# Performance work log

Hardware: AMD Instinct MI355X
Metric: run time of the kernel (lower is better)

Reference implementation:

```python
import jax, jax.numpy as jnp
import numpy as np

B, S, D, H, DFF = 8, 1024, 1024, 16, 4096
DK = D // H
EPS = 1e-6
NEG = -1e9


def setup_inputs() -> dict:
    key = jax.random.key(0)
    ks = jax.random.split(key, 8)
    x = jax.random.normal(ks[0], (B, S, D), dtype=jnp.float32)
    mask = jnp.ones((B, 1, 1, S), dtype=jnp.int32)
    s = 0.02
    wq = jax.random.normal(ks[1], (D, D), jnp.float32) * s
    wk = jax.random.normal(ks[2], (D, D), jnp.float32) * s
    wv = jax.random.normal(ks[3], (D, D), jnp.float32) * s
    wo = jax.random.normal(ks[4], (D, D), jnp.float32) * s
    bq = jnp.zeros((D,), jnp.float32); bk = jnp.zeros((D,), jnp.float32)
    bv = jnp.zeros((D,), jnp.float32); bo = jnp.zeros((D,), jnp.float32)
    w1 = jax.random.normal(ks[5], (D, DFF), jnp.float32) * s
    b1 = jnp.zeros((DFF,), jnp.float32)
    w2 = jax.random.normal(ks[6], (DFF, D), jnp.float32) * s
    b2 = jnp.zeros((D,), jnp.float32)
    g1 = jnp.array(1.0, jnp.float32); be1 = jnp.array(0.0, jnp.float32)
    g2 = jnp.array(1.0, jnp.float32); be2 = jnp.array(0.0, jnp.float32)
    return dict(x=x, mask=mask, wq=wq, bq=bq, wk=wk, bk=bk, wv=wv, bv=bv,
                wo=wo, bo=bo, w1=w1, b1=b1, w2=w2, b2=b2,
                g1=g1, be1=be1, g2=g2, be2=be2)


def layer_norm(x, gamma, beta):
    # repo quirk: unbiased std (ddof=1), scalar gamma/beta, divide by (std+eps)
    mean = jnp.mean(x, axis=-1, keepdims=True)
    std = jnp.std(x, axis=-1, keepdims=True, ddof=1)
    return gamma * (x - mean) / (std + EPS) + beta


def mha(x, mask, wq, bq, wk, bk, wv, bv, wo, bo):
    q = (x @ wq + bq).reshape(B, S, H, DK).transpose(0, 2, 1, 3)  # bhsd
    k = (x @ wk + bk).reshape(B, S, H, DK).transpose(0, 2, 1, 3)
    v = (x @ wv + bv).reshape(B, S, H, DK).transpose(0, 2, 1, 3)
    scores = jnp.einsum('bhqd,bhkd->bhqk', q, k) / jnp.sqrt(jnp.float32(DK))
    scores = jnp.where(mask == 0, NEG, scores)
    attn = jax.nn.softmax(scores, axis=-1)
    out = jnp.einsum('bhqk,bhkd->bhqd', attn, v)
    out = out.transpose(0, 2, 1, 3).reshape(B, S, D)
    return out @ wo + bo


def reference(x, mask, wq, bq, wk, bk, wv, bv, wo, bo, w1, b1, w2, b2, g1, be1, g2, be2):
    # pre-LN residual: x + sublayer(norm(x)); dropout inert at eval
    x = x + mha(layer_norm(x, g1, be1), mask, wq, bq, wk, bk, wv, bv, wo, bo)
    h = layer_norm(x, g2, be2)
    x = x + (jax.nn.relu(h @ w1 + b1) @ w2 + b2)
    return x
```

## Files before the change

### kernel.cpp

```cpp
#include <hip/hip_runtime.h>
#include <math.h>

typedef __bf16 bf16;
typedef float f32x4 __attribute__((ext_vector_type(4)));
typedef float f32x16 __attribute__((ext_vector_type(16)));
typedef bf16 bf16x8 __attribute__((ext_vector_type(8)));
typedef bf16 bf16x4 __attribute__((ext_vector_type(4)));
typedef unsigned int u32;
typedef unsigned int u32x2 __attribute__((ext_vector_type(2)));

#define DEV __device__ __forceinline__

constexpr int Ss = 1024, Dd = 1024;
constexpr float EPSf = 1e-6f;
constexpr float SM_SCALE = 0.125f * 1.4426950408889634f;

DEV void gl_lds16(const void* g, void* l) {
  __builtin_amdgcn_global_load_lds(
      (const __attribute__((address_space(1))) void*)g,
      (__attribute__((address_space(3))) void*)l, 16, 0, 0);
}

DEV u32 cvtpk(float lo, float hi) {
  u32 r;
  asm("v_cvt_pk_bf16_f32 %0, %1, %2" : "=v"(r) : "v"(lo), "v"(hi));
  return r;
}

__global__ __launch_bounds__(256) void prep_k(
    const float* __restrict__ i0, const float* __restrict__ i1,
    const float* __restrict__ i2, const float* __restrict__ i3,
    const float* __restrict__ i4, const float* __restrict__ i5,
    bf16* __restrict__ o0, bf16* __restrict__ o1, bf16* __restrict__ o2,
    bf16* __restrict__ o3, bf16* __restrict__ o4, bf16* __restrict__ o5,
    const float* __restrict__ xin, bf16* __restrict__ lnout,
    const float* __restrict__ gp, const float* __restrict__ bp) {
  const int bi = blockIdx.x;
  const int tid = threadIdx.x;
  if (bi >= 3072) {
    const int row = bi - 3072;
    float v[4];
    const float* p = xin + (size_t)row * Dd + tid * 4;
#pragma unroll
    for (int i = 0; i < 4; i++) v[i] = p[i];
    float s = v[0] + v[1] + v[2] + v[3];
    float s2 = v[0] * v[0] + v[1] * v[1] + v[2] * v[2] + v[3] * v[3];
#pragma unroll
    for (int m = 1; m < 64; m <<= 1) {
      s += __shfl_xor(s, m, 64);
      s2 += __shfl_xor(s2, m, 64);
    }
    __shared__ float ls[4], ls2[4];
    if ((tid & 63) == 0) {
      ls[tid >> 6] = s;
      ls2[tid >> 6] = s2;
    }
    __syncthreads();
    s = ls[0] + ls[1] + ls[2] + ls[3];
    s2 = ls2[0] + ls2[1] + ls2[2] + ls2[3];
    float mean = s * (1.0f / Dd);
    float var = (s2 - (float)Dd * mean * mean) * (1.0f / (Dd - 1));
    var = fmaxf(var, 0.0f);
    float g = gp[0], be = bp[0];
    float rs = g / (sqrtf(var) + EPSf);
    bf16* q = lnout + (size_t)row * Dd + tid * 4;
#pragma unroll
    for (int i = 0; i < 4; i++) q[i] = (bf16)((v[i] - mean) * rs + be);
    return;
  }
  __shared__ float t[64 * 65];
  const float* in;
  bf16* out;
  int R, C, local, sh;
  if (bi < 1024) {
    const int j = bi >> 8;
    local = bi & 255; R = 1024; C = 1024; sh = 4;
    in = (j == 0) ? i0 : (j == 1) ? i1 : (j == 2) ? i2 : i3;
    out = (j == 0) ? o0 : (j == 1) ? o1 : (j == 2) ? o2 : o3;
  } else if (bi < 2048) {
    local = bi - 1024; R = 1024; C = 4096; sh = 6; in = i4; out = o4;
  } else {
    local = bi - 2048; R = 4096; C = 1024; sh = 4; in = i5; out = o5;
  }
  const int nx = 1 << sh;
  const int bx = local & (nx - 1), by = local >> sh;
  const int tx = tid & 63, ty = tid >> 6;
  const int r0 = by * 64, c0 = bx * 64;
#pragma unroll
  for (int i = 0; i < 16; i++) {
    int r = ty + i * 4;
    t[r * 65 + tx] = in[(size_t)(r0 + r) * C + c0 + tx];
  }
  __syncthreads();
#pragma unroll
  for (int i = 0; i < 16; i++) {
    int r = ty + i * 4;
    out[(size_t)(c0 + r) * R + r0 + tx] = (bf16)t[tx * 65 + r];
  }
}

__global__ __launch_bounds__(256) void ln_kernel(
    const float* __restrict__ in, bf16* __restrict__ out,
    const float* __restrict__ gp, const float* __restrict__ bp) {
  const int row = blockIdx.x;
  const int tid = threadIdx.x;
  float v[4];
  const float* p = in + (size_t)row * Dd + tid * 4;
#pragma unroll
  for (int i = 0; i < 4; i++) v[i] = p[i];
  float s = v[0] + v[1] + v[2] + v[3];
  float s2 = v[0] * v[0] + v[1] * v[1] + v[2] * v[2] + v[3] * v[3];
#pragma unroll
  for (int m = 1; m < 64; m <<= 1) {
    s += __shfl_xor(s, m, 64);
    s2 += __shfl_xor(s2, m, 64);
  }
  __shared__ float ls[4], ls2[4];
  if ((tid & 63) == 0) {
    ls[tid >> 6] = s;
    ls2[tid >> 6] = s2;
  }
  __syncthreads();
  s = ls[0] + ls[1] + ls[2] + ls[3];
  s2 = ls2[0] + ls2[1] + ls2[2] + ls2[3];
  float mean = s * (1.0f / Dd);
  float var = (s2 - (float)Dd * mean * mean) * (1.0f / (Dd - 1));
  var = fmaxf(var, 0.0f);
  float g = gp[0], be = bp[0];
  float rs = g / (sqrtf(var) + EPSf);
  bf16* q = out + (size_t)row * Dd + tid * 4;
#pragma unroll
  for (int i = 0; i < 4; i++) q[i] = (bf16)((v[i] - mean) * rs + be);
}

template <int EPI, int BK>
__global__ __launch_bounds__(256) void gemm_bt(
    const bf16* __restrict__ A, const bf16* __restrict__ Bt,
    const float* __restrict__ bias, const float* __restrict__ bias2,
    const float* __restrict__ bias3, const float* __restrict__ resid,
    bf16* __restrict__ vtb, void* __restrict__ Cout, int M, int N, int K,
    int sa, int sb) {
  __shared__ __attribute__((aligned(16))) char smem[2 * 128 * BK * 2];
  bf16* As = (bf16*)smem;
  bf16* Bs = (bf16*)(smem + 128 * BK * 2);
  constexpr int CPR = BK / 8;
  constexpr int RPJ = 256 / CPR;
  constexpr int NJ = BK / 16;
  const int tid = threadIdx.x;
  const int ln = tid & 63;
  const int wv = tid >> 6;
  const int wm = wv >> 1, wn = wv & 1;
  const int quad = ln >> 4, l16 = ln & 15;
  const int l7 = l16 & 7;
  const int nxg = gridDim.x;
  const int d = blockIdx.y * nxg + blockIdx.x;
  const int sseq = d >> 3;
  const int bxr = sseq % nxg;
  const int byr = (d & 7) + 8 * (sseq / nxg);
  const int m0 = byr * 128, n0 = bxr * 128;

  f32x4 acc[4][4];
#pragma unroll
  for (int i = 0; i < 4; i++)
#pragma unroll
    for (int j = 0; j < 4; j++) acc[i][j] = {0.f, 0.f, 0.f, 0.f};

  const int sr = tid / CPR;
  const int sc = (tid & (CPR - 1)) ^ (sr & 7);
  const size_t abase = (size_t)(m0 + sr) * sa + sc * 8;
  const size_t bbase = (size_t)(n0 + sr) * sb + sc * 8;

  for (int k0 = 0; k0 < K; k0 += BK) {
#pragma unroll
    for (int j = 0; j < NJ; j++) {
      gl_lds16(A + abase + (size_t)(j * RPJ) * sa + k0,
               (char*)As + j * 4096 + wv * 1024);
      gl_lds16(Bt + bbase + (size_t)(j * RPJ) * sb + k0,
               (char*)Bs + j * 4096 + wv * 1024);
    }
    __syncthreads();
#pragma unroll
    for (int kh = 0; kh < BK / 32; kh++) {
      bf16x8 af[4], bfr[4];
#pragma unroll
      for (int mi = 0; mi < 4; mi++)
        af[mi] = *(const bf16x8*)&As[(wm * 64 + mi * 16 + l16) * BK +
                                     ((kh * 4 + quad) ^ l7) * 8];
#pragma unroll
      for (int ni = 0; ni < 4; ni++)
        bfr[ni] = *(const bf16x8*)&Bs[(wn * 64 + ni * 16 + l16) * BK +
                                      ((kh * 4 + quad) ^ l7) * 8];
#pragma unroll
      for (int mi = 0; mi < 4; mi++)
#pragma unroll
        for (int ni = 0; ni < 4; ni++)
          acc[mi][ni] = __builtin_amdgcn_mfma_f32_16x16x32_bf16(
              af[mi], bfr[ni], acc[mi][ni], 0, 0, 0);
    }
    __syncthreads();
  }

  if constexpr (EPI == 4) {
    if (n0 < 2048) {
#pragma unroll
      for (int mi = 0; mi < 4; mi++) {
        const int m = m0 + wm * 64 + mi * 16 + quad * 4;
#pragma unroll
        for (int ni = 0; ni < 4; ni++) {
          const int n = n0 + wn * 64 + ni * 16 + l16;
          const float bvl = (n < 1024) ? bias[n] : bias2[n - 1024];
#pragma unroll
          for (int r = 0; r < 4; r++)
            ((bf16*)Cout)[(size_t)(m + r) * N + n] =
                (bf16)(acc[mi][ni][r] + bvl);
        }
      }
    } else {
      bf16* T = (bf16*)smem;
#pragma unroll
      for (int mi = 0; mi < 4; mi++) {
        const int ml = wm * 64 + mi * 16 + quad * 4;
        const int c = ml >> 3, hf = (ml >> 2) & 1;
#pragma unroll
        for (int ni = 0; ni < 4; ni++) {
          const int nl = wn * 64 + ni * 16 + l16;
          const float bvl = bias3[(n0 - 2048) + nl];
          bf16x4 tv;
#pragma unroll
          for (int r = 0; r < 4; r++) tv[r] = (bf16)(acc[mi][ni][r] + bvl);
          *(bf16x4*)&T[nl * 128 + ((c ^ (nl & 15)) << 3) + (hf << 2)] = tv;
        }
      }
      __syncthreads();
      const size_t vbase =
          ((size_t)(m0 >> 10) * 1024 + (n0 - 2048)) * Ss + (m0 & 1023);
#pragma unroll
      for (int p = 0; p < 8; p++) {
        const int row = p * 16 + (tid >> 4);
        const int k = tid & 15;
        bf16x8 vv = *(const bf16x8*)&T[row * 128 + ((k ^ (row & 15)) << 3)];
        *(bf16x8*)&vtb[vbase + (size_t)row * Ss + k * 8] = vv;
      }
    }
  } else {
#pragma unroll
    for (int mi = 0; mi < 4; mi++) {
      const int m = m0 + wm * 64 + mi * 16 + quad * 4;
#pragma unroll
      for (int ni = 0; ni < 4; ni++) {
        const int n = n0 + wn * 64 + ni * 16 + l16;
        float bvl = 0.0f;
        if constexpr (EPI != 3) bvl = bias[n];
#pragma unroll
        for (int r = 0; r < 4; r++) {
          float val = acc[mi][ni][r] + bvl;
          const size_t idx = (size_t)(m + r) * N + n;
          if constexpr (EPI == 1) {
            ((float*)Cout)[idx] = val + resid[idx];
          } else if constexpr (EPI == 2) {
            ((bf16*)Cout)[idx] = (bf16)fmaxf(val, 0.0f);
          } else {
            ((float*)Cout)[idx] = val + resid[idx];
          }
        }
      }
    }
  }
}

__global__ __launch_bounds__(512) void gemm256_relu(
    const bf16* __restrict__ A, const bf16* __restrict__ Bt,
    const float* __restrict__ bias, bf16* __restrict__ Cout, int M, int N,
    int K, int sa, int sb) {
  __shared__ __attribute__((aligned(16))) char smem[131072];
  const int tid = threadIdx.x;
  const int ln = tid & 63;
  const int wv = tid >> 6;
  const int wm = wv >> 2, wn = wv & 3;
  const int quad = ln >> 4, l16 = ln & 15;
  const int l7 = l16 & 7;
  const int nxg = gridDim.x;
  const int d = blockIdx.y * nxg + blockIdx.x;
  const int sseq = d >> 3;
  const int bxr = sseq % nxg;
  const int byr = (d & 7) + 8 * (sseq / nxg);
  const int m0 = byr * 256, n0 = bxr * 256;

  f32x4 acc[8][4];
#pragma unroll
  for (int i = 0; i < 8; i++)
#pragma unroll
    for (int j = 0; j < 4; j++) acc[i][j] = {0.f, 0.f, 0.f, 0.f};

  const int sr = tid >> 3;
  const int sc = (tid & 7) ^ (sr & 7);
  const size_t abase = (size_t)(m0 + sr) * sa + sc * 8;
  const size_t bbase = (size_t)(n0 + sr) * sb + sc * 8;
  const int w8 = tid >> 6;

  const int nt = K >> 6;
  int cur = 0;

  {
#pragma unroll
    for (int j = 0; j < 4; j++) {
      gl_lds16(A + abase + (size_t)(j * 64) * sa,
               smem + j * 8192 + w8 * 1024);
      gl_lds16(Bt + bbase + (size_t)(j * 64) * sb,
               smem + 32768 + j * 8192 + w8 * 1024);
    }
  }
  asm volatile("s_waitcnt vmcnt(0)" ::: "memory");
  __builtin_amdgcn_s_barrier();

  for (int t = 0; t < nt; ++t) {
    const bf16* As = (const bf16*)(smem + cur * 65536);
    const bf16* Bs = (const bf16*)(smem + cur * 65536 + 32768);
    char* ldst = smem + (cur ^ 1) * 65536;
    const bool pf = (t + 1 < nt);
    const int koff = (t + 1) * 64;

    bf16x8 af0[4][2], af1[4][2], bfr[2][2];

#pragma unroll
    for (int mf = 0; mf < 4; mf++)
#pragma unroll
      for (int kh = 0; kh < 2; kh++)
        af0[mf][kh] = *(const bf16x8*)&As[(wm * 128 + mf * 16 + l16) * 64 +
                                          (((kh * 4 + quad) ^ l7) * 8)];
#pragma unroll
    for (int nf = 0; nf < 2; nf++)
#pragma unroll
      for (int kh = 0; kh < 2; kh++)
        bfr[nf][kh] = *(const bf16x8*)&Bs[(wn * 64 + nf * 16 + l16) * 64 +
                                          (((kh * 4 + quad) ^ l7) * 8)];
    if (pf) {
      gl_lds16(Bt + bbase + koff, ldst + 32768 + w8 * 1024);
      gl_lds16(Bt + bbase + (size_t)64 * sb + koff,
               ldst + 32768 + 8192 + w8 * 1024);
    }
    __builtin_amdgcn_s_barrier();
    __builtin_amdgcn_s_setprio(1);
#pragma unroll
    for (int kh = 0; kh < 2; kh++)
#pragma unroll
      for (int mf = 0; mf < 4; mf++)
#pragma unroll
        for (int nf = 0; nf < 2; nf++)
          acc[mf][nf] = __builtin_amdgcn_mfma_f32_16x16x32_bf16(
              af0[mf][kh], bfr[nf][kh], acc[mf][nf], 0, 0, 0);
    __builtin_amdgcn_s_setprio(0);
    if (pf) {
      asm volatile("s_waitcnt vmcnt(2)" ::: "memory");
    } else {
      asm volatile("s_waitcnt vmcnt(0)" ::: "memory");
    }
    __builtin_amdgcn_s_barrier();

#pragma unroll
    for (int mf = 0; mf < 4; mf++)
#pragma unroll
      for (int kh = 0; kh < 2; kh++)
        af1[mf][kh] =
            *(const bf16x8*)&As[(wm * 128 + 64 + mf * 16 + l16) * 64 +
                                (((kh * 4 + quad) ^ l7) * 8)];
    if (pf) {
      gl_lds16(Bt + bbase + (size_t)128 * sb + koff,
               ldst + 32768 + 16384 + w8 * 1024);
      gl_lds16(Bt + bbase + (size_t)192 * sb + koff,
               ldst + 32768 + 24576 + w8 * 1024);
    }
    __builtin_amdgcn_s_barrier();
    __builtin_amdgcn_s_setprio(1);
#pragma unroll
    for (int kh = 0; kh < 2; kh++)
#pragma unroll
      for (int mf = 0; mf < 4; mf++)
#pragma unroll
        for (int nf = 0; nf < 2; nf++)
          acc[4 + mf][nf] = __builtin_amdgcn_mfma_f32_16x16x32_bf16(
              af1[mf][kh], bfr[nf][kh], acc[4 + mf][nf], 0, 0, 0);
    __builtin_amdgcn_s_setprio(0);
    __builtin_amdgcn_s_barrier();

#pragma unroll
    for (int nf = 0; nf < 2; nf++)
#pragma unroll
      for (int kh = 0; kh < 2; kh++)
        bfr[nf][kh] =
            *(const bf16x8*)&Bs[(wn * 64 + 32 + nf * 16 + l16) * 64 +
                                (((kh * 4 + quad) ^ l7) * 8)];
    if (pf) {
      gl_lds16(A + abase + koff, ldst + w8 * 1024);
      gl_lds16(A + abase + (size_t)128 * sa + koff,
               ldst + 16384 + w8 * 1024);
    }
    __builtin_amdgcn_s_barrier();
    __builtin_amdgcn_s_setprio(1);
#pragma unroll
    for (int kh = 0; kh < 2; kh++)
#pragma unroll
      for (int mf = 0; mf < 4; mf++)
#pragma unroll
        for (int nf = 0; nf < 2; nf++)
          acc[4 + mf][2 + nf] = __builtin_amdgcn_mfma_f32_16x16x32_bf16(
              af1[mf][kh], bfr[nf][kh], acc[4 + mf][2 + nf], 0, 0, 0);
    __builtin_amdgcn_s_setprio(0);
    __builtin_amdgcn_s_barrier();

    if (pf) {
      gl_lds16(A + abase + (size_t)64 * sa + koff, ldst + 8192 + w8 * 1024);
      gl_lds16(A + abase + (size_t)192 * sa + koff,
               ldst + 24576 + w8 * 1024);
    }
    __builtin_amdgcn_s_barrier();
    __builtin_amdgcn_s_setprio(1);
#pragma unroll
    for (int kh = 0; kh < 2; kh++)
#pragma unroll
      for (int mf = 0; mf < 4; mf++)
#pragma unroll
        for (int nf = 0; nf < 2; nf++)
          acc[mf][2 + nf] = __builtin_amdgcn_mfma_f32_16x16x32_bf16(
              af0[mf][kh], bfr[nf][kh], acc[mf][2 + nf], 0, 0, 0);
    __builtin_amdgcn_s_setprio(0);
    if (pf) {
      asm volatile("s_waitcnt vmcnt(2)" ::: "memory");
    } else {
      asm volatile("s_waitcnt vmcnt(0)" ::: "memory");
    }
    __builtin_amdgcn_s_barrier();
    cur ^= 1;
  }

#pragma unroll
  for (int mi = 0; mi < 8; mi++) {
    const int m = m0 + wm * 128 + mi * 16 + quad * 4;
#pragma unroll
    for (int ni = 0; ni < 4; ni++) {
      const int n = n0 + wn * 64 + ni * 16 + l16;
      const float bvl = bias[n];
#pragma unroll
      for (int r = 0; r < 4; r++)
        Cout[(size_t)(m + r) * N + n] =
            (bf16)fmaxf(acc[mi][ni][r] + bvl, 0.0f);
    }
  }
}

__global__ __launch_bounds__(256) void attn_k(
    const bf16* __restrict__ qkv, const bf16* __restrict__ vt,
    const int* __restrict__ mask, bf16* __restrict__ ctx) {
  __shared__ __attribute__((aligned(16))) char smem[36864];
  __shared__ int Ft[16];
  bf16* Qs = (bf16*)smem;
  bf16* Ks = (bf16*)(smem + 16384);
  bf16* Vs = (bf16*)(smem + 24576);
  float* Fm = (float*)(smem + 32768);
  const int tid = threadIdx.x;
  const int l = tid & 63, w = tid >> 6;
  const int lq = l & 31, lh = l >> 5;
  const int lq7 = lq & 7;
  const int bh = blockIdx.x;
  const int b = bh >> 4, h = bh & 15;
  const int q0 = blockIdx.y * 128;
  const int sr = tid >> 3;
  const int sc = (tid & 7) ^ (sr & 7);

  if (tid < 16) Ft[tid] = 0;
  {
#pragma unroll
    for (int j = 0; j < 4; j++) {
      const size_t ga =
          (size_t)(b * Ss + q0 + j * 32 + sr) * 3072 + h * 64 + sc * 8;
      gl_lds16(qkv + ga, (char*)Qs + j * 4096 + w * 1024);
    }
  }
  __syncthreads();

  bf16x8 qf[4];
#pragma unroll
  for (int s = 0; s < 4; s++)
    qf[s] =
        *(const bf16x8*)&Qs[(w * 32 + lq) * 64 + (((s * 2 + lh) ^ lq7) * 8)];

  {
    const int4 mv = *(const int4*)&mask[b * Ss + tid * 4];
    const float ninf = -__builtin_inff();
    Fm[tid * 4 + 0] = mv.x ? 0.0f : ninf;
    Fm[tid * 4 + 1] = mv.y ? 0.0f : ninf;
    Fm[tid * 4 + 2] = mv.z ? 0.0f : ninf;
    Fm[tid * 4 + 3] = mv.w ? 0.0f : ninf;
    if (!(mv.x && mv.y && mv.z && mv.w)) atomicOr(&Ft[tid >> 4], 1);
  }

  f32x16 oacc[2];
#pragma unroll
  for (int d = 0; d < 2; d++)
#pragma unroll
    for (int r = 0; r < 16; r++) oacc[d][r] = 0.0f;
  float rsum = 0.0f;

  for (int kk0 = 0; kk0 < Ss; kk0 += 64) {
    {
#pragma unroll
      for (int j = 0; j < 2; j++) {
        const size_t ga = (size_t)(b * Ss + kk0 + j * 32 + sr) * 3072 + 1024 +
                          h * 64 + sc * 8;
        gl_lds16(qkv + ga, (char*)Ks + j * 4096 + w * 1024);
        const size_t gv = (size_t)(bh * 64 + j * 32 + sr) * Ss + kk0 + sc * 8;
        gl_lds16(vt + gv, (char*)Vs + j * 4096 + w * 1024);
      }
    }
    __syncthreads();

    f32x16 sacc[2];
#pragma unroll
    for (int kb = 0; kb < 2; kb++)
#pragma unroll
      for (int r = 0; r < 16; r++) sacc[kb][r] = 0.0f;

    __builtin_amdgcn_s_setprio(1);
#pragma unroll
    for (int kb = 0; kb < 2; kb++)
#pragma unroll
      for (int s = 0; s < 4; s++) {
        const bf16x8 kf = *(const bf16x8*)&Ks[(kb * 32 + lq) * 64 +
                                              (((s * 2 + lh) ^ lq7) * 8)];
        sacc[kb] = __builtin_amdgcn_mfma_f32_32x32x16_bf16(kf, qf[s],
                                                           sacc[kb], 0, 0, 0);
      }
    __builtin_amdgcn_s_setprio(0);

    if (__builtin_amdgcn_readfirstlane(Ft[kk0 >> 6])) {
#pragma unroll
      for (int kb = 0; kb < 2; kb++)
#pragma unroll
        for (int g = 0; g < 4; g++) {
          const f32x4 mv = *(const f32x4*)&Fm[kk0 + kb * 32 + 4 * lh + 8 * g];
#pragma unroll
          for (int j = 0; j < 4; j++)
            sacc[kb][g * 4 + j] = __builtin_amdgcn_exp2f(
                fmaf(sacc[kb][g * 4 + j], SM_SCALE, mv[j]));
        }
    } else {
#pragma unroll
      for (int kb = 0; kb < 2; kb++)
#pragma unroll
        for (int r = 0; r < 16; r++)
          sacc[kb][r] = __builtin_amdgcn_exp2f(sacc[kb][r] * SM_SCALE);
    }
#pragma unroll
    for (int kb = 0; kb < 2; kb++) {
      const float t0 = (sacc[kb][0] + sacc[kb][1]) + (sacc[kb][2] + sacc[kb][3]);
      const float t1 = (sacc[kb][4] + sacc[kb][5]) + (sacc[kb][6] + sacc[kb][7]);
      const float t2 =
          (sacc[kb][8] + sacc[kb][9]) + (sacc[kb][10] + sacc[kb][11]);
      const float t3 =
          (sacc[kb][12] + sacc[kb][13]) + (sacc[kb][14] + sacc[kb][15]);
      rsum += ((t0 + t1) + (t2 + t3));
    }

    __builtin_amdgcn_s_setprio(1);
#pragma unroll
    for (int t = 0; t < 4; t++) {
      const int kb = t >> 1, rb = (t & 1) * 8;
      u32 pa = cvtpk(sacc[kb][rb + 0], sacc[kb][rb + 1]);
      u32 pbv = cvtpk(sacc[kb][rb + 2], sacc[kb][rb + 3]);
      u32 pc = cvtpk(sacc[kb][rb + 4], sacc[kb][rb + 5]);
      u32 pd = cvtpk(sacc[kb][rb + 6], sacc[kb][rb + 7]);
      asm("v_permlane32_swap_b32 %0, %1" : "+v"(pa), "+v"(pc));
      asm("v_permlane32_swap_b32 %0, %1" : "+v"(pbv), "+v"(pd));
      union {
        u32 u[4];
        bf16x8 v;
      } pk;
      pk.u[0] = pa;
      pk.u[1] = pbv;
      pk.u[2] = pc;
      pk.u[3] = pd;
      const int vsw = ((t * 2 + lh) ^ lq7) * 8;
      const bf16x8 vf0 = *(const bf16x8*)&Vs[lq * 64 + vsw];
      const bf16x8 vf1 = *(const bf16x8*)&Vs[(32 + lq) * 64 + vsw];
      oacc[0] =
          __builtin_amdgcn_mfma_f32_32x32x16_bf16(vf0, pk.v, oacc[0], 0, 0, 0);
      oacc[1] =
          __builtin_amdgcn_mfma_f32_32x32x16_bf16(vf1, pk.v, oacc[1], 0, 0, 0);
    }
    __builtin_amdgcn_s_setprio(0);
    __syncthreads();
  }

  float xs = rsum, ys = rsum;
  asm("v_permlane32_swap_b32 %0, %1" : "+v"(xs), "+v"(ys));
  const float inv = 1.0f / (xs + ys);

  bf16* Tb = (bf16*)(smem + w * 4608);
#pragma unroll
  for (int dblk = 0; dblk < 2; dblk++)
#pragma unroll
    for (int g = 0; g < 4; g++) {
      const u32 lo =
          cvtpk(oacc[dblk][g * 4 + 0] * inv, oacc[dblk][g * 4 + 1] * inv);
      const u32 hi =
          cvtpk(oacc[dblk][g * 4 + 2] * inv, oacc[dblk][g * 4 + 3] * inv);
      u32x2 pr2;
      pr2[0] = lo;
      pr2[1] = hi;
      const int dbase = dblk * 32 + 8 * g + 4 * lh;
      *(u32x2*)&Tb[lq * 72 + dbase] = pr2;
    }
  __syncthreads();
#pragma unroll
  for (int p = 0; p < 4; p++) {
    const int row = p * 8 + (l >> 3);
    const int ch = l & 7;
    const bf16x8 vv = *(const bf16x8*)&Tb[row * 72 + ch * 8];
    *(bf16x8*)&ctx[(size_t)(b * Ss + q0 + w * 32 + row) * Dd + h * 64 +
                   ch * 8] = vv;
  }
}

extern "C" void kernel_launch(void* const* d_in, const int* in_sizes, int n_in,
                              void* d_out, int out_size, void* d_ws,
                              size_t ws_size, hipStream_t stream) {
  (void)in_sizes; (void)n_in; (void)out_size;
  const float* x = (const float*)d_in[0];
  const int* mask = (const int*)d_in[1];
  const float* wq = (const float*)d_in[2];
  const float* bq = (const float*)d_in[3];
  const float* wk = (const float*)d_in[4];
  const float* bk = (const float*)d_in[5];
  const float* wvw = (const float*)d_in[6];
  const float* bv = (const float*)d_in[7];
  const float* wo = (const float*)d_in[8];
  const float* bo = (const float*)d_in[9];
  const float* w1 = (const float*)d_in[10];
  const float* b1 = (const float*)d_in[11];
  const float* w2 = (const float*)d_in[12];
  const float* b2 = (const float*)d_in[13];
  const float* g1 = (const float*)d_in[14];
  const float* be1 = (const float*)d_in[15];
  const float* g2 = (const float*)d_in[16];
  const float* be2 = (const float*)d_in[17];
  float* out = (float*)d_out;

  char* ws = (char*)d_ws;
  const size_t MB = 1024 * 1024;
  bf16* w1T = (bf16*)(ws + 0 * MB);
  bf16* w2T = (bf16*)(ws + 8 * MB);
  bf16* wqkvT = (bf16*)(ws + 16 * MB);
  bf16* woT = (bf16*)(ws + 22 * MB);
  bf16* lnb = (bf16*)(ws + 24 * MB);
  bf16* qkv = (bf16*)(ws + 40 * MB);
  bf16* vtb = (bf16*)(ws + 88 * MB);
  float* x1 = (float*)(ws + 40 * MB);
  bf16* ctx = lnb;

  dim3 blk(256);
  prep_k<<<3072 + 8192, blk, 0, stream>>>(
      wq, wk, wvw, wo, w1, w2, wqkvT, wqkvT + (size_t)1024 * 1024,
      wqkvT + (size_t)2048 * 1024, woT, w1T, w2T, x, lnb, g1, be1);
  gemm_bt<4, 64><<<dim3(24, 64), blk, 0, stream>>>(
      lnb, wqkvT, bq, bk, bv, nullptr, vtb, qkv, 8192, 3072, 1024, 1024, 1024);
  attn_k<<<dim3(128, 8), blk, 0, stream>>>(qkv, vtb, mask, ctx);
  gemm_bt<1, 128><<<dim3(8, 64), blk, 0, stream>>>(
      ctx, woT, bo, nullptr, nullptr, x, nullptr, x1, 8192, 1024, 1024, 1024,
      1024);
  ln_kernel<<<8192, blk, 0, stream>>>(x1, lnb, g2, be2);

  if (ws_size >= 136 * MB) {
    bf16* mid = (bf16*)(ws + 72 * MB);
    gemm256_relu<<<dim3(16, 32), dim3(512), 0, stream>>>(
        lnb, w1T, b1, mid, 8192, 4096, 1024, 1024, 1024);
    gemm_bt<1, 128><<<dim3(8, 64), blk, 0, stream>>>(
        mid, w2T, b2, nullptr, nullptr, x1, nullptr, out, 8192, 1024, 4096,
        4096, 4096);
  } else {
    bf16* mid = (bf16*)(ws + 72 * MB);
    gemm256_relu<<<dim3(8, 32), dim3(512), 0, stream>>>(
        lnb, w1T, b1, mid, 8192, 2048, 1024, 1024, 1024);
    gemm_bt<1, 128><<<dim3(8, 64), blk, 0, stream>>>(
        mid, w2T, b2, nullptr, nullptr, x1, nullptr, out, 8192, 1024, 2048,
        2048, 4096);
    gemm256_relu<<<dim3(8, 32), dim3(512), 0, stream>>>(
        lnb, w1T + (size_t)2048 * 1024, b1 + 2048, mid, 8192, 2048, 1024,
        1024, 1024);
    gemm_bt<3, 128><<<dim3(8, 64), blk, 0, stream>>>(
        mid, w2T + 2048, nullptr, nullptr, nullptr, out, nullptr, out, 8192,
        1024, 2048, 2048, 4096);
  }
}
```

Before: 453.6 us.

## Double-buffer K/V tiles in attention and store residual stream in bf16

```diff
diff --git a/kernel.cpp b/kernel.cpp
--- a/kernel.cpp
+++ b/kernel.cpp
@@ -99,15 +99,15 @@
   }
 }
 
-__global__ __launch_bounds__(256) void ln_kernel(
-    const float* __restrict__ in, bf16* __restrict__ out,
+__global__ __launch_bounds__(256) void ln_bf16_k(
+    const bf16* __restrict__ in, bf16* __restrict__ out,
     const float* __restrict__ gp, const float* __restrict__ bp) {
   const int row = blockIdx.x;
   const int tid = threadIdx.x;
+  const bf16x4 vv = *(const bf16x4*)(in + (size_t)row * Dd + tid * 4);
   float v[4];
-  const float* p = in + (size_t)row * Dd + tid * 4;
-#pragma unroll
-  for (int i = 0; i < 4; i++) v[i] = p[i];
+#pragma unroll
+  for (int i = 0; i < 4; i++) v[i] = (float)vv[i];
   float s = v[0] + v[1] + v[2] + v[3];
   float s2 = v[0] * v[0] + v[1] * v[1] + v[2] * v[2] + v[3] * v[3];
 #pragma unroll
@@ -138,8 +138,8 @@
     const bf16* __restrict__ A, const bf16* __restrict__ Bt,
     const float* __restrict__ bias, const float* __restrict__ bias2,
     const float* __restrict__ bias3, const float* __restrict__ resid,
-    bf16* __restrict__ vtb, void* __restrict__ Cout, int M, int N, int K,
-    int sa, int sb) {
+    const bf16* __restrict__ vtbr, bf16* __restrict__ vtb,
+    void* __restrict__ Cout, int M, int N, int K, int sa, int sb) {
   __shared__ __attribute__((aligned(16))) char smem[2 * 128 * BK * 2];
   bf16* As = (bf16*)smem;
   bf16* Bs = (bf16*)(smem + 128 * BK * 2);
@@ -259,8 +259,12 @@
             ((float*)Cout)[idx] = val + resid[idx];
           } else if constexpr (EPI == 2) {
             ((bf16*)Cout)[idx] = (bf16)fmaxf(val, 0.0f);
+          } else if constexpr (EPI == 3) {
+            ((float*)Cout)[idx] = val + resid[idx];
+          } else if constexpr (EPI == 5) {
+            ((bf16*)Cout)[idx] = (bf16)(val + resid[idx]);
           } else {
-            ((float*)Cout)[idx] = val + resid[idx];
+            ((float*)Cout)[idx] = val + (float)vtbr[idx];
           }
         }
       }
@@ -454,8 +458,6 @@
   __shared__ __attribute__((aligned(16))) char smem[36864];
   __shared__ int Ft[16];
   bf16* Qs = (bf16*)smem;
-  bf16* Ks = (bf16*)(smem + 16384);
-  bf16* Vs = (bf16*)(smem + 24576);
   float* Fm = (float*)(smem + 32768);
   const int tid = threadIdx.x;
   const int l = tid & 63, w = tid >> 6;
@@ -473,17 +475,17 @@
     for (int j = 0; j < 4; j++) {
       const size_t ga =
           (size_t)(b * Ss + q0 + j * 32 + sr) * 3072 + h * 64 + sc * 8;
-      gl_lds16(qkv + ga, (char*)Qs + j * 4096 + w * 1024);
-    }
-  }
-  __syncthreads();
-
-  bf16x8 qf[4];
-#pragma unroll
-  for (int s = 0; s < 4; s++)
-    qf[s] =
-        *(const bf16x8*)&Qs[(w * 32 + lq) * 64 + (((s * 2 + lh) ^ lq7) * 8)];
-
+      gl_lds16(qkv + ga, smem + j * 4096 + w * 1024);
+    }
+#pragma unroll
+    for (int j = 0; j < 2; j++) {
+      const size_t ga =
+          (size_t)(b * Ss + j * 32 + sr) * 3072 + 1024 + h * 64 + sc * 8;
+      gl_lds16(qkv + ga, smem + 16384 + j * 4096 + w * 1024);
+      const size_t gv = (size_t)(bh * 64 + j * 32 + sr) * Ss + sc * 8;
+      gl_lds16(vt + gv, smem + 24576 + j * 4096 + w * 1024);
+    }
+  }
   {
     const int4 mv = *(const int4*)&mask[b * Ss + tid * 4];
     const float ninf = -__builtin_inff();
@@ -493,6 +495,14 @@
     Fm[tid * 4 + 3] = mv.w ? 0.0f : ninf;
     if (!(mv.x && mv.y && mv.z && mv.w)) atomicOr(&Ft[tid >> 4], 1);
   }
+  __syncthreads();
+
+  bf16x8 qf[4];
+#pragma unroll
+  for (int s = 0; s < 4; s++)
+    qf[s] =
+        *(const bf16x8*)&Qs[(w * 32 + lq) * 64 + (((s * 2 + lh) ^ lq7) * 8)];
+  __syncthreads();
 
   f32x16 oacc[2];
 #pragma unroll
@@ -501,18 +511,27 @@
     for (int r = 0; r < 16; r++) oacc[d][r] = 0.0f;
   float rsum = 0.0f;
 
-  for (int kk0 = 0; kk0 < Ss; kk0 += 64) {
-    {
+  for (int t = 0; t < 16; ++t) {
+    const int kk0 = t * 64;
+    if (t + 1 < 16) {
+      char* dst = smem + (((t + 1) & 1) ? 0 : 16384);
+      const int nk = kk0 + 64;
 #pragma unroll
       for (int j = 0; j < 2; j++) {
-        const size_t ga = (size_t)(b * Ss + kk0 + j * 32 + sr) * 3072 + 1024 +
-                          h * 64 + sc * 8;
-        gl_lds16(qkv + ga, (char*)Ks + j * 4096 + w * 1024);
-        const size_t gv = (size_t)(bh * 64 + j * 32 + sr) * Ss + kk0 + sc * 8;
-        gl_lds16(vt + gv, (char*)Vs + j * 4096 + w * 1024);
+        const size_t ga =
+            (size_t)(b * Ss + nk + j * 32 + sr) * 3072 + 1024 + h * 64 +
+            sc * 8;
+        gl_lds16(qkv + ga, dst + j * 4096 + w * 1024);
+        const size_t gv = (size_t)(bh * 64 + j * 32 + sr) * Ss + nk + sc * 8;
+        gl_lds16(vt + gv, dst + 8192 + j * 4096 + w * 1024);
       }
-    }
-    __syncthreads();
+      asm volatile("s_waitcnt vmcnt(4)" ::: "memory");
+    } else {
+      asm volatile("s_waitcnt vmcnt(0)" ::: "memory");
+    }
+    __builtin_amdgcn_s_barrier();
+    const bf16* Ks = (const bf16*)(smem + ((t & 1) ? 0 : 16384));
+    const bf16* Vs = Ks + 4096;
 
     f32x16 sacc[2];
 #pragma unroll
@@ -532,7 +551,7 @@
       }
     __builtin_amdgcn_s_setprio(0);
 
-    if (__builtin_amdgcn_readfirstlane(Ft[kk0 >> 6])) {
+    if (__builtin_amdgcn_readfirstlane(Ft[t])) {
 #pragma unroll
       for (int kb = 0; kb < 2; kb++)
 #pragma unroll
@@ -563,8 +582,8 @@
 
     __builtin_amdgcn_s_setprio(1);
 #pragma unroll
-    for (int t = 0; t < 4; t++) {
-      const int kb = t >> 1, rb = (t & 1) * 8;
+    for (int tt = 0; tt < 4; tt++) {
+      const int kb = tt >> 1, rb = (tt & 1) * 8;
       u32 pa = cvtpk(sacc[kb][rb + 0], sacc[kb][rb + 1]);
       u32 pbv = cvtpk(sacc[kb][rb + 2], sacc[kb][rb + 3]);
       u32 pc = cvtpk(sacc[kb][rb + 4], sacc[kb][rb + 5]);
@@ -579,7 +598,7 @@
       pk.u[1] = pbv;
       pk.u[2] = pc;
       pk.u[3] = pd;
-      const int vsw = ((t * 2 + lh) ^ lq7) * 8;
+      const int vsw = ((tt * 2 + lh) ^ lq7) * 8;
       const bf16x8 vf0 = *(const bf16x8*)&Vs[lq * 64 + vsw];
       const bf16x8 vf1 = *(const bf16x8*)&Vs[(32 + lq) * 64 + vsw];
       oacc[0] =
@@ -588,7 +607,8 @@
           __builtin_amdgcn_mfma_f32_32x32x16_bf16(vf1, pk.v, oacc[1], 0, 0, 0);
     }
     __builtin_amdgcn_s_setprio(0);
-    __syncthreads();
+    asm volatile("s_waitcnt lgkmcnt(0)" ::: "memory");
+    __builtin_amdgcn_s_barrier();
   }
 
   float xs = rsum, ys = rsum;
@@ -654,7 +674,7 @@
   bf16* lnb = (bf16*)(ws + 24 * MB);
   bf16* qkv = (bf16*)(ws + 40 * MB);
   bf16* vtb = (bf16*)(ws + 88 * MB);
-  float* x1 = (float*)(ws + 40 * MB);
+  bf16* x1b = (bf16*)(ws + 40 * MB);
   bf16* ctx = lnb;
 
   dim3 blk(256);
@@ -662,32 +682,33 @@
       wq, wk, wvw, wo, w1, w2, wqkvT, wqkvT + (size_t)1024 * 1024,
       wqkvT + (size_t)2048 * 1024, woT, w1T, w2T, x, lnb, g1, be1);
   gemm_bt<4, 64><<<dim3(24, 64), blk, 0, stream>>>(
-      lnb, wqkvT, bq, bk, bv, nullptr, vtb, qkv, 8192, 3072, 1024, 1024, 1024);
+      lnb, wqkvT, bq, bk, bv, nullptr, nullptr, vtb, qkv, 8192, 3072, 1024,
+      1024, 1024);
   attn_k<<<dim3(128, 8), blk, 0, stream>>>(qkv, vtb, mask, ctx);
-  gemm_bt<1, 128><<<dim3(8, 64), blk, 0, stream>>>(
-      ctx, woT, bo, nullptr, nullptr, x, nullptr, x1, 8192, 1024, 1024, 1024,
-      1024);
-  ln_kernel<<<8192, blk, 0, stream>>>(x1, lnb, g2, be2);
+  gemm_bt<5, 128><<<dim3(8, 64), blk, 0, stream>>>(
+      ctx, woT, bo, nullptr, nullptr, x, nullptr, nullptr, x1b, 8192, 1024,
+      1024, 1024, 1024);
+  ln_bf16_k<<<8192, blk, 0, stream>>>(x1b, lnb, g2, be2);
 
   if (ws_size >= 136 * MB) {
     bf16* mid = (bf16*)(ws + 72 * MB);
     gemm256_relu<<<dim3(16, 32), dim3(512), 0, stream>>>(
         lnb, w1T, b1, mid, 8192, 4096, 1024, 1024, 1024);
-    gemm_bt<1, 128><<<dim3(8, 64), blk, 0, stream>>>(
-        mid, w2T, b2, nullptr, nullptr, x1, nullptr, out, 8192, 1024, 4096,
-        4096, 4096);
+    gemm_bt<6, 128><<<dim3(8, 64), blk, 0, stream>>>(
+        mid, w2T, b2, nullptr, nullptr, nullptr, x1b, nullptr, out, 8192,
+        1024, 4096, 4096, 4096);
   } else {
     bf16* mid = (bf16*)(ws + 72 * MB);
     gemm256_relu<<<dim3(8, 32), dim3(512), 0, stream>>>(
         lnb, w1T, b1, mid, 8192, 2048, 1024, 1024, 1024);
-    gemm_bt<1, 128><<<dim3(8, 64), blk, 0, stream>>>(
-        mid, w2T, b2, nullptr, nullptr, x1, nullptr, out, 8192, 1024, 2048,
-        2048, 4096);
+    gemm_bt<6, 128><<<dim3(8, 64), blk, 0, stream>>>(
+        mid, w2T, b2, nullptr, nullptr, nullptr, x1b, nullptr, out, 8192,
+        1024, 2048, 2048, 4096);
     gemm256_relu<<<dim3(8, 32), dim3(512), 0, stream>>>(
         lnb, w1T + (size_t)2048 * 1024, b1 + 2048, mid, 8192, 2048, 1024,
         1024, 1024);
     gemm_bt<3, 128><<<dim3(8, 64), blk, 0, stream>>>(
-        mid, w2T + 2048, nullptr, nullptr, nullptr, out, nullptr, out, 8192,
-        1024, 2048, 2048, 4096);
+        mid, w2T + 2048, nullptr, nullptr, nullptr, out, nullptr, nullptr,
+        out, 8192, 1024, 2048, 2048, 4096);
   }
 }
```

Measured after the change: 441.0 us. -2.8%, faster.
